# Performance work log

Hardware: AMD Instinct MI355X
Metric: run time of the kernel (lower is better)

Reference implementation:

```python
import jax, jax.numpy as jnp
import numpy as np

B, N, S, D, H = 1, 128, 256, 512, 4
DK = D // H
FF = 4 * D

def _ln(x, g, b):
    mu = x.mean(-1, keepdims=True)
    var = x.var(-1, keepdims=True)
    return (x - mu) * jax.lax.rsqrt(var + 1e-6) * g + b

def _triblock_softmax(ld, lu, ll):
    m = jnp.maximum(jnp.maximum(
        jax.lax.stop_gradient(ld.max(-1, keepdims=True)),
        jax.lax.stop_gradient(lu.max(-1, keepdims=True))),
        jax.lax.stop_gradient(ll.max(-1, keepdims=True)))
    ed, eu, el = jnp.exp(ld - m), jnp.exp(lu - m), jnp.exp(ll - m)
    den = ed.sum(-1, keepdims=True) + eu.sum(-1, keepdims=True) + el.sum(-1, keepdims=True)
    return ed / den, eu / den, el / den

def _attn(h, mask, Wq, Wk, Wv, Wo, bo):
    # h: [B, N blocks, S block_size, D]
    q = (h @ Wq).reshape(B, N, S, H, DK)
    k = (h @ Wk).reshape(B, N, S, H, DK)
    v = (h @ Wv).reshape(B, N, S, H, DK)
    k = jnp.pad(k, ((0, 0), (1, 1), (0, 0), (0, 0), (0, 0)))
    v = jnp.pad(v, ((0, 0), (1, 1), (0, 0), (0, 0), (0, 0)))
    scale = DK ** (-0.5)
    qk = lambda kk: jnp.einsum('bnqhd,bnkhd->bnhqk', q, kk) * scale
    ld = jnp.where(mask[:, 0], qk(k[:, 1:-1]), -1e30)  # diag
    lu = jnp.where(mask[:, 1], qk(k[:, 2:]), -1e30)    # upper diag
    ll = jnp.where(mask[:, 2], qk(k[:, :-2]), -1e30)   # lower diag
    wd, wu, wl = _triblock_softmax(ld, lu, ll)
    av = lambda w, vv: jnp.einsum('bnhqk,bnkhd->bnqhd', w, vv)
    o = av(wd, v[:, 1:-1]) + av(wu, v[:, 2:]) + av(wl, v[:, :-2])
    o = o.reshape(B, N, S, H * DK)
    return o @ Wo + bo

def setup_inputs():
    key = jax.random.key(0)
    ks = jax.random.split(key, 8)
    def w(k, shape, fan):
        return jax.random.normal(k, shape, jnp.float32) * np.float32(1.0 / np.sqrt(fan))
    return {
        'x': jax.random.normal(ks[0], (B, N, S, D), jnp.float32),
        'mask': jnp.ones((B, 3, N, 1, S, S), jnp.bool_),
        'Wq': w(ks[1], (D, H * DK), D),
        'Wk': w(ks[2], (D, H * DK), D),
        'Wv': w(ks[3], (D, H * DK), D),
        'Wo': w(ks[4], (H * DK, D), D),
        'bo': jnp.zeros((D,), jnp.float32),
        'W1': w(ks[5], (D, FF), D),
        'b1': jnp.zeros((FF,), jnp.float32),
        'W2': w(ks[6], (FF, D), FF),
        'b2': jnp.zeros((D,), jnp.float32),
        'g1': jnp.ones((D,), jnp.float32),
        'be1': jnp.zeros((D,), jnp.float32),
        'g2': jnp.ones((D,), jnp.float32),
        'be2': jnp.zeros((D,), jnp.float32),
    }

def reference(x, mask, Wq, Wk, Wv, Wo, bo, W1, b1, W2, b2, g1, be1, g2, be2):
    # pre-LN transformer block: x + TriblockdiagMHA(LN(x)); x + FFN(LN(x))
    x = x + _attn(_ln(x, g1, be1), mask, Wq, Wk, Wv, Wo, bo)
    h = _ln(x, g2, be2)
    x = x + (jax.nn.gelu(h @ W1 + b1) @ W2 + b2)
    return x
```

## Files before the change

### kernel.cpp

```cpp
#include <hip/hip_runtime.h>
#include <cstdint>
#include <cstddef>

typedef unsigned short ushort_t;
using bf16x8 = __attribute__((ext_vector_type(8))) short;
using f32x4  = __attribute__((ext_vector_type(4))) float;
using u16x4  = __attribute__((ext_vector_type(4))) unsigned short;

__device__ __forceinline__ ushort_t f2bf(float f) {
    union { float f; unsigned u; } v; v.f = f;
    unsigned r = v.u + 0x7fffu + ((v.u >> 16) & 1u);
    return (ushort_t)(r >> 16);
}

__device__ __forceinline__ void gload_lds16(const void* g, void* l) {
    __builtin_amdgcn_global_load_lds(
        (const __attribute__((address_space(1))) void*)g,
        (__attribute__((address_space(3))) void*)l, 16, 0, 0);
}

__global__ __launch_bounds__(256)
void transpose_f32_bf16(const float* __restrict__ in, ushort_t* __restrict__ out,
                        int R, int C)
{
    __shared__ float tile[32][33];
    int tx = threadIdx.x, ty = threadIdx.y;
    int bx = blockIdx.x, by = blockIdx.y;
    int x = bx * 32 + tx;
    #pragma unroll
    for (int i = 0; i < 32; i += 8)
        tile[ty + i][tx] = in[(size_t)(by * 32 + ty + i) * C + x];
    __syncthreads();
    int xo = by * 32 + tx;
    #pragma unroll
    for (int i = 0; i < 32; i += 8)
        out[(size_t)(bx * 32 + ty + i) * R + xo] = f2bf(tile[tx][ty + i]);
}

__global__ __launch_bounds__(256)
void ln_kernel(const float* __restrict__ x, const float* __restrict__ gg,
               const float* __restrict__ bb, ushort_t* __restrict__ out)
{
    int w = threadIdx.x >> 6, l = threadIdx.x & 63;
    size_t row = (size_t)blockIdx.x * 4 + w;
    const float* xr = x + row * 512;
    f32x4 v0 = *(const f32x4*)&xr[l * 4];
    f32x4 v1 = *(const f32x4*)&xr[256 + l * 4];
    float s1 = v0[0] + v0[1] + v0[2] + v0[3] + v1[0] + v1[1] + v1[2] + v1[3];
    float s2 = v0[0]*v0[0] + v0[1]*v0[1] + v0[2]*v0[2] + v0[3]*v0[3]
             + v1[0]*v1[0] + v1[1]*v1[1] + v1[2]*v1[2] + v1[3]*v1[3];
    #pragma unroll
    for (int m = 1; m < 64; m <<= 1) {
        s1 += __shfl_xor(s1, m, 64);
        s2 += __shfl_xor(s2, m, 64);
    }
    float mean = s1 * (1.0f / 512.0f);
    float var  = s2 * (1.0f / 512.0f) - mean * mean;
    float rs   = rsqrtf(var + 1e-6f);
    f32x4 ga = *(const f32x4*)&gg[l * 4];
    f32x4 gb = *(const f32x4*)&gg[256 + l * 4];
    f32x4 ba = *(const f32x4*)&bb[l * 4];
    f32x4 bv = *(const f32x4*)&bb[256 + l * 4];
    u16x4 o0, o1;
    #pragma unroll
    for (int j = 0; j < 4; ++j) {
        o0[j] = f2bf((v0[j] - mean) * rs * ga[j] + ba[j]);
        o1[j] = f2bf((v1[j] - mean) * rs * gb[j] + bv[j]);
    }
    *(u16x4*)&out[row * 512 + l * 4] = o0;
    *(u16x4*)&out[row * 512 + 256 + l * 4] = o1;
}

template<int EPI>
__global__ __launch_bounds__(256)
void gemm_bt(const ushort_t* __restrict__ A, const ushort_t* __restrict__ BT,
             void* __restrict__ outp, const float* __restrict__ bias,
             const float* __restrict__ resid, int M, int N, int K, int ldc)
{
    __shared__ ushort_t As[128 * 64];
    __shared__ ushort_t Bs[128 * 64];
    const int tid = threadIdx.x;
    const int w = tid >> 6, l = tid & 63, lr = l & 15, lg = l >> 4;
    const int m0 = blockIdx.y * 128, n0 = blockIdx.x * 128;
    const int wm = (w >> 1) * 64, wn = (w & 1) * 64;
    const int erow = tid >> 3;
    const int ecol = (tid & 7) * 8;
    f32x4 acc[4][4] = {};

    for (int k0 = 0; k0 < K; k0 += 64) {
        #pragma unroll
        for (int i = 0; i < 4; ++i) {
            int row = i * 32 + erow;
            gload_lds16(A  + (size_t)(m0 + row) * K + k0 + ecol,
                        (char*)As + i * 4096 + w * 1024);
            gload_lds16(BT + (size_t)(n0 + row) * K + k0 + ecol,
                        (char*)Bs + i * 4096 + w * 1024);
        }
        __syncthreads();
        #pragma unroll
        for (int kk = 0; kk < 2; ++kk) {
            bf16x8 af[4], bfr[4];
            #pragma unroll
            for (int mt = 0; mt < 4; ++mt)
                af[mt] = *(const bf16x8*)&As[(wm + mt * 16 + lr) * 64 + kk * 32 + lg * 8];
            #pragma unroll
            for (int nt = 0; nt < 4; ++nt)
                bfr[nt] = *(const bf16x8*)&Bs[(wn + nt * 16 + lr) * 64 + kk * 32 + lg * 8];
            #pragma unroll
            for (int mt = 0; mt < 4; ++mt)
                #pragma unroll
                for (int nt = 0; nt < 4; ++nt)
                    acc[mt][nt] = __builtin_amdgcn_mfma_f32_16x16x32_bf16(
                        af[mt], bfr[nt], acc[mt][nt], 0, 0, 0);
        }
        __syncthreads();
    }

    #pragma unroll
    for (int mt = 0; mt < 4; ++mt) {
        int rowb = m0 + wm + mt * 16 + lg * 4;
        #pragma unroll
        for (int nt = 0; nt < 4; ++nt) {
            int col = n0 + wn + nt * 16 + lr;
            f32x4 c = acc[mt][nt];
            if (EPI == 0) {
                ushort_t* O = (ushort_t*)outp;
                #pragma unroll
                for (int r = 0; r < 4; ++r)
                    O[(size_t)(rowb + r) * ldc + col] = f2bf(c[r]);
            } else if (EPI == 1) {
                float* O = (float*)outp;
                float bz = bias[col];
                #pragma unroll
                for (int r = 0; r < 4; ++r) {
                    size_t off = (size_t)(rowb + r) * ldc + col;
                    O[off] = resid[off] + c[r] + bz;
                }
            } else {
                ushort_t* O = (ushort_t*)outp;
                float bz = bias[col];
                #pragma unroll
                for (int r = 0; r < 4; ++r) {
                    float t = c[r] + bz;
                    float zh = 0.79788456080286535588f * (t + 0.044715f * t * t * t);
                    float gl = t / (1.0f + __builtin_amdgcn_exp2f(-2.8853900817779268f * zh));
                    O[(size_t)(rowb + r) * ldc + col] = f2bf(gl);
                }
            }
        }
    }
}

__global__ __launch_bounds__(256)
void attn_kernel(const ushort_t* __restrict__ q, const ushort_t* __restrict__ k,
                 const ushort_t* __restrict__ vT, ushort_t* __restrict__ ao)
{
    __shared__ ushort_t P_s[4][32 * 32];
    const int n = blockIdx.x, h = blockIdx.y, z = blockIdx.z;
    const int w = threadIdx.x >> 6, l = threadIdx.x & 63, lr = l & 15, lg = l >> 4;
    const int qrow0 = n * 256 + z * 128 + w * 32;
    const float sc = 0.08838834764831845f * 1.4426950408889634f;

    bf16x8 aq[2][4];
    #pragma unroll
    for (int qt = 0; qt < 2; ++qt)
        #pragma unroll
        for (int kc = 0; kc < 4; ++kc)
            aq[qt][kc] = *(const bf16x8*)&q[(size_t)(qrow0 + qt * 16 + lr) * 1024
                                            + h * 128 + kc * 32 + lg * 8];
    f32x4 o[2][8] = {};
    float dp[2][4] = {};

    for (int d = -1; d <= 1; ++d) {
        int nb = n + d;
        if (nb < 0 || nb > 127) continue;
        for (int t = 0; t < 8; ++t) {
            int j0 = nb * 256 + t * 32;
            f32x4 s[2][2] = {};
            #pragma unroll
            for (int kc = 0; kc < 4; ++kc) {
                #pragma unroll
                for (int kt = 0; kt < 2; ++kt) {
                    bf16x8 kb = *(const bf16x8*)&k[(size_t)(j0 + kt * 16 + lr) * 1024
                                                   + h * 128 + kc * 32 + lg * 8];
                    s[0][kt] = __builtin_amdgcn_mfma_f32_16x16x32_bf16(aq[0][kc], kb, s[0][kt], 0, 0, 0);
                    s[1][kt] = __builtin_amdgcn_mfma_f32_16x16x32_bf16(aq[1][kc], kb, s[1][kt], 0, 0, 0);
                }
            }
            #pragma unroll
            for (int qt = 0; qt < 2; ++qt)
                #pragma unroll
                for (int kt = 0; kt < 2; ++kt)
                    #pragma unroll
                    for (int r = 0; r < 4; ++r) {
                        float p = __builtin_amdgcn_exp2f(s[qt][kt][r] * sc);
                        dp[qt][r] += p;
                        P_s[w][(qt * 16 + lg * 4 + r) * 32 + kt * 16 + lr] = f2bf(p);
                    }
            bf16x8 pa0 = *(const bf16x8*)&P_s[w][(lr) * 32 + lg * 8];
            bf16x8 pa1 = *(const bf16x8*)&P_s[w][(16 + lr) * 32 + lg * 8];
            #pragma unroll
            for (int dt = 0; dt < 8; ++dt) {
                bf16x8 vb = *(const bf16x8*)&vT[(size_t)(h * 128 + dt * 16 + lr) * 32768
                                                 + j0 + lg * 8];
                o[0][dt] = __builtin_amdgcn_mfma_f32_16x16x32_bf16(pa0, vb, o[0][dt], 0, 0, 0);
                o[1][dt] = __builtin_amdgcn_mfma_f32_16x16x32_bf16(pa1, vb, o[1][dt], 0, 0, 0);
            }
        }
    }

    float edge = (n == 0 || n == 127) ? 256.0f : 0.0f;
    #pragma unroll
    for (int qt = 0; qt < 2; ++qt)
        #pragma unroll
        for (int r = 0; r < 4; ++r) {
            float v = dp[qt][r];
            v += __shfl_xor(v, 1, 64);
            v += __shfl_xor(v, 2, 64);
            v += __shfl_xor(v, 4, 64);
            v += __shfl_xor(v, 8, 64);
            dp[qt][r] = v + edge;
        }
    #pragma unroll
    for (int qt = 0; qt < 2; ++qt)
        #pragma unroll
        for (int dt = 0; dt < 8; ++dt)
            #pragma unroll
            for (int r = 0; r < 4; ++r)
                ao[(size_t)(qrow0 + qt * 16 + lg * 4 + r) * 512
                   + h * 128 + dt * 16 + lr] = f2bf(o[qt][dt][r] / dp[qt][r]);
}

extern "C" void kernel_launch(void* const* d_in, const int* in_sizes, int n_in,
                              void* d_out, int out_size, void* d_ws, size_t ws_size,
                              hipStream_t stream)
{
    const float* x   = (const float*)d_in[0];
    const float* Wq  = (const float*)d_in[2];
    const float* Wk  = (const float*)d_in[3];
    const float* Wv  = (const float*)d_in[4];
    const float* Wo  = (const float*)d_in[5];
    const float* bo  = (const float*)d_in[6];
    const float* W1  = (const float*)d_in[7];
    const float* b1  = (const float*)d_in[8];
    const float* W2  = (const float*)d_in[9];
    const float* b2  = (const float*)d_in[10];
    const float* g1  = (const float*)d_in[11];
    const float* be1 = (const float*)d_in[12];
    const float* g2  = (const float*)d_in[13];
    const float* be2 = (const float*)d_in[14];
    float* out = (float*)d_out;

    char* ws = (char*)d_ws;
    const size_t MiB = 1ull << 20;
    ushort_t* WqkT = (ushort_t*)(ws + 0 * MiB);
    ushort_t* WvT  = (ushort_t*)(ws + 1 * MiB);
    ushort_t* WoT  = (ushort_t*)(ws + 1 * MiB + 524288);
    ushort_t* W1T  = (ushort_t*)(ws + 2 * MiB);
    ushort_t* W2T  = (ushort_t*)(ws + 4 * MiB);
    ushort_t* hb   = (ushort_t*)(ws + 8   * MiB);
    ushort_t* qkb  = (ushort_t*)(ws + 40  * MiB);
    ushort_t* vTb  = (ushort_t*)(ws + 104 * MiB);
    ushort_t* aob  = (ushort_t*)(ws + 136 * MiB);
    ushort_t* gbuf = (ushort_t*)(ws + 40  * MiB);

    dim3 tb(32, 8);
    transpose_f32_bf16<<<dim3(16, 16), tb, 0, stream>>>(Wq, WqkT, 512, 512);
    transpose_f32_bf16<<<dim3(16, 16), tb, 0, stream>>>(Wk, WqkT + 262144, 512, 512);
    transpose_f32_bf16<<<dim3(16, 16), tb, 0, stream>>>(Wv, WvT, 512, 512);
    transpose_f32_bf16<<<dim3(16, 16), tb, 0, stream>>>(Wo, WoT, 512, 512);
    transpose_f32_bf16<<<dim3(64, 16), tb, 0, stream>>>(W1, W1T, 512, 2048);
    transpose_f32_bf16<<<dim3(16, 64), tb, 0, stream>>>(W2, W2T, 2048, 512);

    ln_kernel<<<8192, 256, 0, stream>>>(x, g1, be1, hb);

    gemm_bt<0><<<dim3(8, 256), 256, 0, stream>>>(hb, WqkT, qkb, nullptr, nullptr, 32768, 1024, 512, 1024);
    gemm_bt<0><<<dim3(256, 4), 256, 0, stream>>>(WvT, hb, vTb, nullptr, nullptr, 512, 32768, 512, 32768);

    attn_kernel<<<dim3(128, 4, 2), 256, 0, stream>>>(qkb, qkb + 512, vTb, aob);

    gemm_bt<1><<<dim3(4, 256), 256, 0, stream>>>(aob, WoT, out, bo, x, 32768, 512, 512, 512);

    ln_kernel<<<8192, 256, 0, stream>>>(out, g2, be2, hb);

    gemm_bt<2><<<dim3(16, 256), 256, 0, stream>>>(hb, W1T, gbuf, b1, nullptr, 32768, 2048, 512, 2048);

    gemm_bt<1><<<dim3(4, 256), 256, 0, stream>>>(gbuf, W2T, out, b2, out, 32768, 512, 2048, 512);
}
```

Baseline: 796.5 us.

## Use 256x256 GEMM tiles with double-buffered LDS and swizzled layout

Replaces the 128x128 GEMM with a 256x256-tile kernel run by 512 threads, eight waves of which each compute a 128x64 sub-tile. K-slices of 32 are double-buffered in LDS with async global-to-LDS loads issued two stages ahead, and an XOR swizzle is applied to avoid bank conflicts. The aim is more operand reuse per byte loaded and overlap of loads with MFMA work. In exchange the grid has fewer blocks (e.g. 256 for the output projection), which may underfill the CUs, and register pressure is higher.

```diff
diff --git a/kernel.cpp b/kernel.cpp
--- a/kernel.cpp
+++ b/kernel.cpp
@@ -72,56 +72,74 @@
 }
 
 template<int EPI>
-__global__ __launch_bounds__(256)
-void gemm_bt(const ushort_t* __restrict__ A, const ushort_t* __restrict__ BT,
+__global__ __launch_bounds__(512, 2)
+void gemm256(const ushort_t* __restrict__ A, const ushort_t* __restrict__ BT,
              void* __restrict__ outp, const float* __restrict__ bias,
              const float* __restrict__ resid, int M, int N, int K, int ldc)
 {
-    __shared__ ushort_t As[128 * 64];
-    __shared__ ushort_t Bs[128 * 64];
+    __shared__ ushort_t As[2][256 * 32];
+    __shared__ ushort_t Bs[2][256 * 32];
     const int tid = threadIdx.x;
     const int w = tid >> 6, l = tid & 63, lr = l & 15, lg = l >> 4;
-    const int m0 = blockIdx.y * 128, n0 = blockIdx.x * 128;
-    const int wm = (w >> 1) * 64, wn = (w & 1) * 64;
-    const int erow = tid >> 3;
-    const int ecol = (tid & 7) * 8;
-    f32x4 acc[4][4] = {};
-
-    for (int k0 = 0; k0 < K; k0 += 64) {
-        #pragma unroll
-        for (int i = 0; i < 4; ++i) {
-            int row = i * 32 + erow;
-            gload_lds16(A  + (size_t)(m0 + row) * K + k0 + ecol,
-                        (char*)As + i * 4096 + w * 1024);
-            gload_lds16(BT + (size_t)(n0 + row) * K + k0 + ecol,
-                        (char*)Bs + i * 4096 + w * 1024);
-        }
-        __syncthreads();
-        #pragma unroll
-        for (int kk = 0; kk < 2; ++kk) {
-            bf16x8 af[4], bfr[4];
-            #pragma unroll
-            for (int mt = 0; mt < 4; ++mt)
-                af[mt] = *(const bf16x8*)&As[(wm + mt * 16 + lr) * 64 + kk * 32 + lg * 8];
+    const int m0 = blockIdx.y * 256, n0 = blockIdx.x * 256;
+    const int wm = (w >> 2) * 128, wn = (w & 3) * 64;
+
+    f32x4 acc[8][4] = {};
+
+    auto STAGE = [&](int kt, int b) {
+        const int k0 = kt * 32;
+        const int srow = tid >> 2;
+        const int qa = (tid & 3) ^ (srow & 3);
+        #pragma unroll
+        for (int j = 0; j < 2; ++j) {
+            const int row = j * 128 + srow;
+            gload_lds16(A  + (size_t)(m0 + row) * K + k0 + qa * 8,
+                        (char*)&As[b][0] + j * 8192 + tid * 16);
+            gload_lds16(BT + (size_t)(n0 + row) * K + k0 + qa * 8,
+                        (char*)&Bs[b][0] + j * 8192 + tid * 16);
+        }
+    };
+
+    const int nkt = K >> 5;
+    STAGE(0, 0);
+    STAGE(1, 1);
+
+    for (int kt = 0; kt < nkt; ++kt) {
+        const int b = kt & 1;
+        asm volatile("s_waitcnt vmcnt(4)" ::: "memory");
+        __builtin_amdgcn_s_barrier();
+
+        bf16x8 af[8], bfr[4];
+        #pragma unroll
+        for (int mt = 0; mt < 8; ++mt) {
+            const int r = wm + mt * 16 + lr;
+            af[mt] = *(const bf16x8*)&As[b][r * 32 + ((lg ^ (r & 3)) * 8)];
+        }
+        #pragma unroll
+        for (int nt = 0; nt < 4; ++nt) {
+            const int r = wn + nt * 16 + lr;
+            bfr[nt] = *(const bf16x8*)&Bs[b][r * 32 + ((lg ^ (r & 3)) * 8)];
+        }
+        asm volatile("s_waitcnt lgkmcnt(0)" ::: "memory");
+        __builtin_amdgcn_sched_barrier(0);
+        __builtin_amdgcn_s_barrier();
+
+        if (kt + 2 < nkt) STAGE(kt + 2, b);
+
+        #pragma unroll
+        for (int mt = 0; mt < 8; ++mt)
             #pragma unroll
             for (int nt = 0; nt < 4; ++nt)
-                bfr[nt] = *(const bf16x8*)&Bs[(wn + nt * 16 + lr) * 64 + kk * 32 + lg * 8];
-            #pragma unroll
-            for (int mt = 0; mt < 4; ++mt)
-                #pragma unroll
-                for (int nt = 0; nt < 4; ++nt)
-                    acc[mt][nt] = __builtin_amdgcn_mfma_f32_16x16x32_bf16(
-                        af[mt], bfr[nt], acc[mt][nt], 0, 0, 0);
-        }
-        __syncthreads();
-    }
-
-    #pragma unroll
-    for (int mt = 0; mt < 4; ++mt) {
-        int rowb = m0 + wm + mt * 16 + lg * 4;
+                acc[mt][nt] = __builtin_amdgcn_mfma_f32_16x16x32_bf16(
+                    af[mt], bfr[nt], acc[mt][nt], 0, 0, 0);
+    }
+
+    #pragma unroll
+    for (int mt = 0; mt < 8; ++mt) {
+        const int rowb = m0 + wm + mt * 16 + lg * 4;
         #pragma unroll
         for (int nt = 0; nt < 4; ++nt) {
-            int col = n0 + wn + nt * 16 + lr;
+            const int col = n0 + wn + nt * 16 + lr;
             f32x4 c = acc[mt][nt];
             if (EPI == 0) {
                 ushort_t* O = (ushort_t*)outp;
@@ -130,15 +148,15 @@
                     O[(size_t)(rowb + r) * ldc + col] = f2bf(c[r]);
             } else if (EPI == 1) {
                 float* O = (float*)outp;
-                float bz = bias[col];
+                const float bz = bias[col];
                 #pragma unroll
                 for (int r = 0; r < 4; ++r) {
-                    size_t off = (size_t)(rowb + r) * ldc + col;
+                    const size_t off = (size_t)(rowb + r) * ldc + col;
                     O[off] = resid[off] + c[r] + bz;
                 }
             } else {
                 ushort_t* O = (ushort_t*)outp;
-                float bz = bias[col];
+                const float bz = bias[col];
                 #pragma unroll
                 for (int r = 0; r < 4; ++r) {
                     float t = c[r] + bz;
@@ -274,16 +292,16 @@
 
     ln_kernel<<<8192, 256, 0, stream>>>(x, g1, be1, hb);
 
-    gemm_bt<0><<<dim3(8, 256), 256, 0, stream>>>(hb, WqkT, qkb, nullptr, nullptr, 32768, 1024, 512, 1024);
-    gemm_bt<0><<<dim3(256, 4), 256, 0, stream>>>(WvT, hb, vTb, nullptr, nullptr, 512, 32768, 512, 32768);
+    gemm256<0><<<dim3(4, 128), 512, 0, stream>>>(hb, WqkT, qkb, nullptr, nullptr, 32768, 1024, 512, 1024);
+    gemm256<0><<<dim3(128, 2), 512, 0, stream>>>(WvT, hb, vTb, nullptr, nullptr, 512, 32768, 512, 32768);
 
     attn_kernel<<<dim3(128, 4, 2), 256, 0, stream>>>(qkb, qkb + 512, vTb, aob);
 
-    gemm_bt<1><<<dim3(4, 256), 256, 0, stream>>>(aob, WoT, out, bo, x, 32768, 512, 512, 512);
+    gemm256<1><<<dim3(2, 128), 512, 0, stream>>>(aob, WoT, out, bo, x, 32768, 512, 512, 512);
 
     ln_kernel<<<8192, 256, 0, stream>>>(out, g2, be2, hb);
 
-    gemm_bt<2><<<dim3(16, 256), 256, 0, stream>>>(hb, W1T, gbuf, b1, nullptr, 32768, 2048, 512, 2048);
-
-    gemm_bt<1><<<dim3(4, 256), 256, 0, stream>>>(gbuf, W2T, out, b2, out, 32768, 512, 2048, 512);
-}
+    gemm256<2><<<dim3(8, 128), 512, 0, stream>>>(hb, W1T, gbuf, b1, nullptr, 32768, 2048, 512, 2048);
+
+    gemm256<1><<<dim3(2, 128), 512, 0, stream>>>(gbuf, W2T, out, b2, out, 32768, 512, 2048, 512);
+}
```

Result: faster. 768.3 us (-3.5%).
